# Optimization experiments

Measured on AMD Instinct MI355X. Metric: run time of the kernel, lower is better.

The kernel has to match this reference:

```python
import jax, jax.numpy as jnp
import numpy as np
import math

B, S, F, D = 8, 2048, 1024, 1024
NEG = -1e9


def setup_inputs() -> dict:
    key = jax.random.key(0)
    ks = jax.random.split(key, 5)
    x = jax.random.normal(ks[0], (B, S, F), dtype=jnp.float32)
    r_mat = jax.random.normal(ks[1], (B, S, S), dtype=jnp.float32)
    # shared causal attention mask [S, S] (1 = keep, 0 = masked)
    attn_mask = jnp.tril(jnp.ones((S, S), dtype=jnp.float32))
    # per-batch padding mask [B, 1, S]: last 128 tokens of half the batch padded
    pad = jnp.ones((B, 1, S), dtype=jnp.float32)
    pad = pad.at[B // 2:, :, S - 128:].set(0.0)
    Wq = jax.random.normal(ks[2], (F, D), dtype=jnp.float32) / math.sqrt(F)
    Wk = jax.random.normal(ks[3], (F, D), dtype=jnp.float32) / math.sqrt(F)
    Wv = jax.random.normal(ks[4], (F, D), dtype=jnp.float32) / math.sqrt(F)
    return {"x": x, "r_mat": r_mat, "attn_mask": attn_mask, "pad_mask": pad,
            "Wq": Wq, "Wk": Wk, "Wv": Wv}


def reference(x, r_mat, attn_mask, pad_mask, Wq, Wk, Wv):
    scale = math.sqrt(x.shape[-1])  # original scales by sqrt(features)
    q = jnp.einsum('bsf,fd->bsd', x, Wq)
    k = jnp.einsum('bsf,fd->bsd', x, Wk)
    v = jnp.einsum('bsf,fd->bsd', x, Wv)
    scores = jnp.einsum('bsd,btd->bst', q, k) / scale  # [B, S, S]
    keep = (pad_mask != 0.0) & (attn_mask[None] != 0.0)  # [B, S, S] broadcast
    r = jnp.where(keep, r_mat, NEG)
    r = jax.nn.softmax(r, axis=-1)
    scores = jnp.where(keep, scores + r, NEG)
    prob = jax.nn.softmax(scores, axis=-1)
    return jnp.einsum('bst,btd->bsd', prob, v)
```

## Files before the change

### kernel.cpp

```cpp
#include <hip/hip_runtime.h>
#include <hip/hip_bf16.h>

#define B_ 8
#define S_ 2048
#define F_ 1024
#define D_ 1024

typedef unsigned short u16;
typedef float f32x4 __attribute__((ext_vector_type(4)));
typedef __bf16 bf16x8 __attribute__((ext_vector_type(8)));
typedef unsigned short u16x8 __attribute__((ext_vector_type(8)));

__device__ __forceinline__ u16 f2bf(float f) {
  union { float f; unsigned u; } v; v.f = f;
  unsigned r = v.u + 0x7fff + ((v.u >> 16) & 1);
  return (u16)(r >> 16);
}
__device__ __forceinline__ float bf2f(u16 b) {
  union { unsigned u; float f; } v; v.u = ((unsigned)b) << 16;
  return v.f;
}

__device__ __forceinline__ void stage16(const u16* g, u16* l) {
  __builtin_amdgcn_global_load_lds(
      (const __attribute__((address_space(1))) void*)g,
      (__attribute__((address_space(3))) void*)l, 16, 0, 0);
}


__global__ void cast_x(const float* __restrict__ x, u16* __restrict__ xb, int n4) {
  int i = blockIdx.x * blockDim.x + threadIdx.x;
  int stride = gridDim.x * blockDim.x;
  for (; i < n4; i += stride) {
    float4 v = ((const float4*)x)[i];
    ushort4 o;
    o.x = f2bf(v.x); o.y = f2bf(v.y); o.z = f2bf(v.z); o.w = f2bf(v.w);
    ((ushort4*)xb)[i] = o;
  }
}

__global__ void transW(const float* __restrict__ Wq, const float* __restrict__ Wk,
                       const float* __restrict__ Wv, u16* __restrict__ Wt) {
  __shared__ float tile[32][33];
  int z = blockIdx.z;
  const float* W = (z == 0) ? Wq : ((z == 1) ? Wk : Wv);
  int f0 = blockIdx.y * 32, d0 = blockIdx.x * 32;
  int tx = threadIdx.x & 31, ty = threadIdx.x >> 5;
  for (int i = 0; i < 4; i++)
    tile[ty + i * 8][tx] = W[(size_t)(f0 + ty + i * 8) * D_ + d0 + tx];
  __syncthreads();
  u16* o = Wt + (size_t)z * D_ * F_;
  for (int i = 0; i < 4; i++)
    o[(size_t)(d0 + ty + i * 8) * F_ + f0 + tx] = f2bf(tile[tx][ty + i * 8]);
}

__global__ __launch_bounds__(256) void r_rowsum(const float* __restrict__ r,
                                                const float* __restrict__ pm,
                                                float* __restrict__ rs) {
  int row = blockIdx.x;
  int b = row >> 11, s = row & 2047;
  const float4* rp = (const float4*)(r + (size_t)row * S_);
  const float4* pp = (const float4*)(pm + (size_t)b * S_);
  int nv = (s >> 2) + 1;
  float acc = 0.f;
  for (int i = threadIdx.x; i < nv; i += 256) {
    float4 rv = rp[i];
    float4 pv = pp[i];
    int t0 = i << 2;
    #pragma unroll
    for (int j = 0; j < 4; j++) {
      int t = t0 + j;
      if (t <= s && (&pv.x)[j] != 0.f) acc += __expf((&rv.x)[j] - 16.f);
    }
  }
  for (int off = 1; off < 64; off <<= 1) acc += __shfl_xor(acc, off);
  __shared__ float wsum[4];
  int lane = threadIdx.x & 63, w = threadIdx.x >> 6;
  if (lane == 0) wsum[w] = acc;
  __syncthreads();
  if (threadIdx.x == 0) rs[row] = wsum[0] + wsum[1] + wsum[2] + wsum[3];
}


__device__ __forceinline__ void stageA(const u16* __restrict__ src, int ld, int h,
                                       u16* ldsA, int w, int l) {
  int base = ((w >> 2) * 128) + h * 64 + ((w & 3) * 16);
  int r = l >> 3, ch = (l & 7) ^ (l >> 3);
  #pragma unroll
  for (int i = 0; i < 2; i++) {
    int row = base + i * 8;
    stage16(src + (size_t)(row + r) * ld + ch * 8, ldsA + row * 64);
  }
}
__device__ __forceinline__ void stageB(const u16* __restrict__ src, int ld, int h,
                                       u16* ldsB, int w, int l) {
  int base = h * 128 + w * 16;
  int r = l >> 3, ch = (l & 7) ^ (l >> 3);
  #pragma unroll
  for (int i = 0; i < 2; i++) {
    int row = base + i * 8;
    stage16(src + (size_t)(row + r) * ld + ch * 8, ldsB + row * 64);
  }
}

__device__ __forceinline__ bf16x8 readfrag(const u16* lds, int row, int ks, int hi) {
  int c = ((ks << 6) + (hi << 4)) ^ ((row & 7) << 4);
  return *(const bf16x8*)((const char*)lds + row * 128 + c);
}

#define MFMA_QUAD(MB, KB)                                                        \
  __builtin_amdgcn_s_setprio(1);                                                 \
  _Pragma("unroll")                                                              \
  for (int m = 0; m < 4; m++)                                                    \
    _Pragma("unroll")                                                            \
    for (int n = 0; n < 4; n++)                                                  \
      acc[(MB) + m][n] = __builtin_amdgcn_mfma_f32_16x16x32_bf16(                \
          af[m], bfr[(KB) + n], acc[(MB) + m][n], 0, 0, 0);                      \
  __builtin_amdgcn_s_setprio(0);

#define SYNC_POINT()                                                             \
  __builtin_amdgcn_sched_barrier(0);                                             \
  __builtin_amdgcn_s_barrier();                                                  \
  __builtin_amdgcn_sched_barrier(0);

__device__ __forceinline__ void gemm256(const u16* __restrict__ A, int lda,
                                        const u16* __restrict__ B, int ldb,
                                        int nT, u16* lds, f32x4 acc[8][4]) {
  const int t = threadIdx.x, w = t >> 6, l = t & 63;
  const int wr = w >> 2, wc = w & 3;
  u16* A0 = lds;           u16* B0 = lds + 16384;
  u16* A1 = lds + 32768;   u16* B1 = lds + 49152;

  #pragma unroll
  for (int m = 0; m < 8; m++)
    #pragma unroll
    for (int n = 0; n < 4; n++)
      #pragma unroll
      for (int j = 0; j < 4; j++) acc[m][n][j] = 0.f;

  stageB(B, ldb, 0, B0, w, l);
  stageB(B, ldb, 1, B0, w, l);
  stageA(A, lda, 0, A0, w, l);
  stageA(A, lda, 1, A0, w, l);
  if (nT > 1) stageA(A + 64, lda, 0, A1, w, l);
  asm volatile("s_waitcnt vmcnt(4)" ::: "memory");
  SYNC_POINT()

  const int arow = wr * 128 + (l & 15), brow = wc * 64 + (l & 15), hi = l >> 4;

  for (int kt = 0; kt < nT; kt++) {
    u16* cA = (kt & 1) ? A1 : A0;
    u16* cB = (kt & 1) ? B1 : B0;
    u16* nA = (kt & 1) ? A0 : A1;
    u16* nB = (kt & 1) ? B0 : B1;
    const u16* An1 = A + (size_t)(kt + 1) * 64;
    const u16* Bn1 = B + (size_t)(kt + 1) * 64;
    const u16* An2 = A + (size_t)(kt + 2) * 64;
    const bool has1 = (kt + 1 < nT), has2 = (kt + 2 < nT);
    bf16x8 af[4], bfr[8];

    #pragma unroll
    for (int m = 0; m < 4; m++) af[m] = readfrag(cA, arow + m * 16, 0, hi);
    #pragma unroll
    for (int n = 0; n < 4; n++) bfr[n] = readfrag(cB, brow + n * 16, 0, hi);
    if (has1) stageB(Bn1, ldb, 0, nB, w, l);
    MFMA_QUAD(0, 0)

    #pragma unroll
    for (int m = 0; m < 4; m++) af[m] = readfrag(cA, arow + m * 16, 1, hi);
    #pragma unroll
    for (int n = 0; n < 4; n++) bfr[4 + n] = readfrag(cB, brow + n * 16, 1, hi);
    if (has1) {
      stageB(Bn1, ldb, 1, nB, w, l);
      asm volatile("s_waitcnt vmcnt(4)" ::: "memory");
    } else {
      asm volatile("s_waitcnt vmcnt(0)" ::: "memory");
    }
    SYNC_POINT()
    MFMA_QUAD(0, 4)

    #pragma unroll
    for (int m = 0; m < 4; m++) af[m] = readfrag(cA, arow + 64 + m * 16, 0, hi);
    if (has2) stageA(An2, lda, 0, cA, w, l);
    MFMA_QUAD(4, 0)

    #pragma unroll
    for (int m = 0; m < 4; m++) af[m] = readfrag(cA, arow + 64 + m * 16, 1, hi);
    if (has1) stageA(An1, lda, 1, nA, w, l);
    if (has1 && has2)  { asm volatile("s_waitcnt vmcnt(4)" ::: "memory"); }
    else if (has1)     { asm volatile("s_waitcnt vmcnt(2)" ::: "memory"); }
    else               { asm volatile("s_waitcnt vmcnt(0)" ::: "memory"); }
    SYNC_POINT()
    MFMA_QUAD(4, 4)
  }
}

__device__ __forceinline__ void store256_bf16(f32x4 acc[8][4], u16* smem,
                                              u16* dst, int ld) {
  int t = threadIdx.x, w = t >> 6, l = t & 63;
  int wr = w >> 2, wc = w & 3;
  #pragma unroll
  for (int q = 0; q < 4; q++) {
    __syncthreads();
    if (wr == (q >> 1)) {
      int mb = (q & 1) * 4;
      #pragma unroll
      for (int mm = 0; mm < 4; mm++)
        #pragma unroll
        for (int j = 0; j < 4; j++) {
          int row = mm * 16 + (l >> 4) * 4 + j;
          #pragma unroll
          for (int n = 0; n < 4; n++)
            smem[row * 264 + wc * 64 + n * 16 + (l & 15)] = f2bf(acc[mb + mm][n][j]);
        }
    }
    __syncthreads();
    #pragma unroll
    for (int i = 0; i < 4; i++) {
      int idx = i * 512 + t;
      int row = idx >> 5, ch = idx & 31;
      *(u16x8*)(dst + (size_t)(q * 64 + row) * ld + ch * 8) =
          *(const u16x8*)(smem + row * 264 + ch * 8);
    }
  }
}

__global__ __launch_bounds__(512, 2) void gemm_qkv(
    const u16* __restrict__ xb, const u16* __restrict__ Wt,
    u16* __restrict__ qb, u16* __restrict__ kb, u16* __restrict__ vT) {
  __shared__ __align__(16) u16 lds[65536];
  int z = blockIdx.z;
  f32x4 acc[8][4];
  if (z < 2) {
    int m0 = blockIdx.x * 256, n0 = blockIdx.y * 256;
    gemm256(xb + (size_t)m0 * F_, F_,
            Wt + (size_t)z * D_ * F_ + (size_t)n0 * F_, F_, F_ / 64, lds, acc);
    store256_bf16(acc, lds, ((z == 0) ? qb : kb) + (size_t)m0 * D_ + n0, D_);
  } else {
    int d0 = blockIdx.y * 256, s0g = blockIdx.x * 256;
    gemm256(Wt + 2ULL * D_ * F_ + (size_t)d0 * F_, F_,
            xb + (size_t)s0g * F_, F_, F_ / 64, lds, acc);
    int b = s0g >> 11, s0 = s0g & 2047;
    store256_bf16(acc, lds, vT + (size_t)b * D_ * S_ + (size_t)d0 * S_ + s0, S_);
  }
}

__global__ __launch_bounds__(512, 2) void attn_scores(
    const u16* __restrict__ qb, const u16* __restrict__ kb,
    const float* __restrict__ r_mat, const float* __restrict__ pm,
    const float* __restrict__ rs_r, u16* __restrict__ P,
    float* __restrict__ rowsum) {
  int mt = blockIdx.x, nt = blockIdx.y, b = blockIdx.z;
  if (nt > mt) return;
  __shared__ __align__(16) u16 lds[65536];
  int m0 = mt * 256, n0 = nt * 256;
  f32x4 acc[8][4];
  gemm256(qb + ((size_t)b * S_ + m0) * D_, D_,
          kb + ((size_t)b * S_ + n0) * D_, D_, D_ / 64, lds, acc);
  int t = threadIdx.x, w = t >> 6, l = t & 63;
  int wr = w >> 2, wc = w & 3;
  float* fs = (float*)lds;
  const float* rb = r_mat + (size_t)b * S_ * S_;
  const float* pmp = pm + (size_t)b * S_ + n0;
  #pragma unroll
  for (int q = 0; q < 4; q++) {
    __syncthreads();
    if (wr == (q >> 1)) {
      int mb = (q & 1) * 4;
      #pragma unroll
      for (int mm = 0; mm < 4; mm++)
        #pragma unroll
        for (int j = 0; j < 4; j++) {
          int row = mm * 16 + (l >> 4) * 4 + j;
          #pragma unroll
          for (int n = 0; n < 4; n++)
            fs[row * 260 + wc * 64 + n * 16 + (l & 15)] = acc[mb + mm][n][j];
        }
    }
    __syncthreads();
    int row = t >> 3, cg = t & 7;
    int srow = m0 + q * 64 + row;
    float invr = 1.f / rs_r[b * S_ + srow];
    const float* rrow = rb + (size_t)srow * S_ + n0 + cg * 32;
    u16* prow = P + (size_t)b * S_ * S_ + (size_t)srow * S_ + n0 + cg * 32;
    const float* fsc = fs + row * 260 + cg * 32;
    float rsum = 0.f;
    #pragma unroll
    for (int cc = 0; cc < 4; cc++) {
      int ch = (cg + cc) & 3;
      f32x4 q0 = *(const f32x4*)(fsc + ch * 8);
      f32x4 q1 = *(const f32x4*)(fsc + ch * 8 + 4);
      f32x4 r0 = *(const f32x4*)(rrow + ch * 8);
      f32x4 r1 = *(const f32x4*)(rrow + ch * 8 + 4);
      f32x4 p0 = *(const f32x4*)(pmp + cg * 32 + ch * 8);
      f32x4 p1 = *(const f32x4*)(pmp + cg * 32 + ch * 8 + 4);
      u16x8 o;
      #pragma unroll
      for (int k = 0; k < 8; k++) {
        int tc = n0 + cg * 32 + ch * 8 + k;
        float rv = (k < 4) ? r0[k] : r1[k - 4];
        float pmv = (k < 4) ? p0[k] : p1[k - 4];
        float qk = (k < 4) ? q0[k] : q1[k - 4];
        bool keep = (tc <= srow) && (pmv != 0.f);
        float rsm = __expf(rv - 16.f) * invr;
        float e = keep ? __expf(fmaf(qk, 0.03125f, rsm - 16.f)) : 0.f;
        u16 pb = f2bf(e); o[k] = pb; rsum += bf2f(pb);
      }
      *(u16x8*)(prow + ch * 8) = o;
    }
    for (int off = 1; off < 8; off <<= 1) rsum += __shfl_xor(rsum, off);
    if ((t & 7) == 0) atomicAdd(&rowsum[b * S_ + srow], rsum);
  }
}

__global__ __launch_bounds__(512, 2) void attn_pv(
    const u16* __restrict__ P, const u16* __restrict__ vT,
    const float* __restrict__ rowsum, float* __restrict__ out) {
  __shared__ __align__(16) u16 lds[65536];
  int mt = blockIdx.x, dt = blockIdx.y, b = blockIdx.z;
  int m0 = mt * 256, n0 = dt * 256;
  int kmax = m0 + 256;
  f32x4 acc[8][4];
  gemm256(P + ((size_t)b * S_ + m0) * S_, S_,
          vT + ((size_t)b * D_ + n0) * S_, S_, kmax / 64, lds, acc);
  int t = threadIdx.x, w = t >> 6, l = t & 63;
  int wr = w >> 2, wc = w & 3;
  float* fs = (float*)lds;
  #pragma unroll
  for (int q = 0; q < 4; q++) {
    __syncthreads();
    if (wr == (q >> 1)) {
      int mb = (q & 1) * 4;
      #pragma unroll
      for (int mm = 0; mm < 4; mm++)
        #pragma unroll
        for (int j = 0; j < 4; j++) {
          int row = mm * 16 + (l >> 4) * 4 + j;
          float inv = 1.f / rowsum[b * S_ + m0 + q * 64 + row];
          #pragma unroll
          for (int n = 0; n < 4; n++)
            fs[row * 260 + wc * 64 + n * 16 + (l & 15)] = acc[mb + mm][n][j] * inv;
        }
    }
    __syncthreads();
    #pragma unroll
    for (int i = 0; i < 8; i++) {
      int idx = i * 512 + t;
      int row = idx >> 6, c4 = (idx & 63) << 2;
      *(float4*)(out + ((size_t)b * S_ + m0 + q * 64 + row) * D_ + n0 + c4) =
          *(const float4*)(fs + row * 260 + c4);
    }
  }
}

extern "C" void kernel_launch(void* const* d_in, const int* in_sizes, int n_in,
                              void* d_out, int out_size, void* d_ws, size_t ws_size,
                              hipStream_t stream) {
  const float* x     = (const float*)d_in[0];
  const float* r_mat = (const float*)d_in[1];
  const float* pm    = (const float*)d_in[3];
  const float* Wq    = (const float*)d_in[4];
  const float* Wk    = (const float*)d_in[5];
  const float* Wv    = (const float*)d_in[6];
  float* out = (float*)d_out;
  char* ws = (char*)d_ws;

  u16*   qb     = (u16*)(ws + 0);
  u16*   kb     = (u16*)(ws + 33554432ULL);
  u16*   vT     = (u16*)(ws + 67108864ULL);
  float* rs_r   = (float*)(ws + 100663296ULL);
  float* rowsum = (float*)(ws + 100728832ULL);
  u16*   P      = (u16*)(ws + 100794368ULL);
  u16*   xb     = (u16*)(ws + 100794368ULL);
  u16*   Wt     = (u16*)(ws + 134348800ULL);

  cast_x<<<dim3(2048), dim3(256), 0, stream>>>(x, xb, (B_ * S_ * F_) / 4);
  transW<<<dim3(32, 32, 3), dim3(256), 0, stream>>>(Wq, Wk, Wv, Wt);
  r_rowsum<<<dim3(B_ * S_), dim3(256), 0, stream>>>(r_mat, pm, rs_r);
  gemm_qkv<<<dim3(64, 4, 3), dim3(512), 0, stream>>>(xb, Wt, qb, kb, vT);
  hipMemsetAsync(rowsum, 0, B_ * S_ * sizeof(float), stream);
  attn_scores<<<dim3(8, 8, 8), dim3(512), 0, stream>>>(qb, kb, r_mat, pm, rs_r, P, rowsum);
  attn_pv<<<dim3(8, 4, 8), dim3(512), 0, stream>>>(P, vT, rowsum, out);
}
```

Before: 306.7 us.

## Switch attention kernels to 128x128 tiles with triangular-only grid and heavy-first ordering

Adds a 128x128 GEMM core with 256 threads and uses it in attn_scores and attn_pv in place of the 256x256 tiles. attn_scores now launches only the lower-triangular tiles through a linear index decoded with sqrt, so no blocks exit early. Finer tiles cut wasted causal work on the diagonal and give more blocks per GPU. attn_pv is ordered so the longest rows start first. In exchange there is less operand reuse per tile and more global traffic and atomics.

```diff
diff --git a/kernel.cpp b/kernel.cpp
--- a/kernel.cpp
+++ b/kernel.cpp
@@ -82,6 +82,17 @@
 }
 
 
+__device__ __forceinline__ bf16x8 readfrag(const u16* lds, int row, int ks, int hi) {
+  int c = ((ks << 6) + (hi << 4)) ^ ((row & 7) << 4);
+  return *(const bf16x8*)((const char*)lds + row * 128 + c);
+}
+
+#define SYNC_POINT()                                                             \
+  __builtin_amdgcn_sched_barrier(0);                                             \
+  __builtin_amdgcn_s_barrier();                                                  \
+  __builtin_amdgcn_sched_barrier(0);
+
+
 __device__ __forceinline__ void stageA(const u16* __restrict__ src, int ld, int h,
                                        u16* ldsA, int w, int l) {
   int base = ((w >> 2) * 128) + h * 64 + ((w & 3) * 16);
@@ -101,11 +112,6 @@
     int row = base + i * 8;
     stage16(src + (size_t)(row + r) * ld + ch * 8, ldsB + row * 64);
   }
-}
-
-__device__ __forceinline__ bf16x8 readfrag(const u16* lds, int row, int ks, int hi) {
-  int c = ((ks << 6) + (hi << 4)) ^ ((row & 7) << 4);
-  return *(const bf16x8*)((const char*)lds + row * 128 + c);
 }
 
 #define MFMA_QUAD(MB, KB)                                                        \
@@ -117,11 +123,6 @@
       acc[(MB) + m][n] = __builtin_amdgcn_mfma_f32_16x16x32_bf16(                \
           af[m], bfr[(KB) + n], acc[(MB) + m][n], 0, 0, 0);                      \
   __builtin_amdgcn_s_setprio(0);
-
-#define SYNC_POINT()                                                             \
-  __builtin_amdgcn_sched_barrier(0);                                             \
-  __builtin_amdgcn_s_barrier();                                                  \
-  __builtin_amdgcn_sched_barrier(0);
 
 __device__ __forceinline__ void gemm256(const u16* __restrict__ A, int lda,
                                         const u16* __restrict__ B, int ldb,
@@ -245,45 +246,134 @@
   }
 }
 
-__global__ __launch_bounds__(512, 2) void attn_scores(
+
+__device__ __forceinline__ void stage128(const u16* __restrict__ src, int ld, int h,
+                                         u16* ldsT, int w, int l) {
+  int base = h * 64 + w * 16;
+  int r = l >> 3, ch = (l & 7) ^ (l >> 3);
+  #pragma unroll
+  for (int i = 0; i < 2; i++) {
+    int row = base + i * 8;
+    stage16(src + (size_t)(row + r) * ld + ch * 8, ldsT + row * 64);
+  }
+}
+
+#define MFMA16(AF, BF)                                                           \
+  __builtin_amdgcn_s_setprio(1);                                                 \
+  _Pragma("unroll")                                                              \
+  for (int m = 0; m < 4; m++)                                                    \
+    _Pragma("unroll")                                                            \
+    for (int n = 0; n < 4; n++)                                                  \
+      acc[m][n] = __builtin_amdgcn_mfma_f32_16x16x32_bf16(                       \
+          AF[m], BF[n], acc[m][n], 0, 0, 0);                                     \
+  __builtin_amdgcn_s_setprio(0);
+
+__device__ __forceinline__ void gemm128(const u16* __restrict__ A, int lda,
+                                        const u16* __restrict__ B, int ldb,
+                                        int nT, u16* lds, f32x4 acc[4][4]) {
+  const int t = threadIdx.x, w = t >> 6, l = t & 63;
+  const int wr = w >> 1, wc = w & 1;
+  u16* A0 = lds;          u16* B0 = lds + 8192;
+  u16* A1 = lds + 16384;  u16* B1 = lds + 24576;
+
+  #pragma unroll
+  for (int m = 0; m < 4; m++)
+    #pragma unroll
+    for (int n = 0; n < 4; n++)
+      #pragma unroll
+      for (int j = 0; j < 4; j++) acc[m][n][j] = 0.f;
+
+  stage128(A, lda, 0, A0, w, l);
+  stage128(A, lda, 1, A0, w, l);
+  stage128(B, ldb, 0, B0, w, l);
+  stage128(B, ldb, 1, B0, w, l);
+  if (nT > 1) {
+    stage128(A + 64, lda, 0, A1, w, l);
+    stage128(A + 64, lda, 1, A1, w, l);
+    asm volatile("s_waitcnt vmcnt(4)" ::: "memory");
+  } else {
+    asm volatile("s_waitcnt vmcnt(0)" ::: "memory");
+  }
+  SYNC_POINT()
+
+  const int arow = wr * 64 + (l & 15), brow = wc * 64 + (l & 15), hi = l >> 4;
+
+  for (int kt = 0; kt < nT; kt++) {
+    u16* cA = (kt & 1) ? A1 : A0;
+    u16* cB = (kt & 1) ? B1 : B0;
+    u16* nB = (kt & 1) ? B0 : B1;
+    const bool has1 = (kt + 1 < nT), has2 = (kt + 2 < nT);
+    bf16x8 a0f[4], b0f[4], a1f[4], b1f[4];
+
+    #pragma unroll
+    for (int m = 0; m < 4; m++) a0f[m] = readfrag(cA, arow + m * 16, 0, hi);
+    #pragma unroll
+    for (int n = 0; n < 4; n++) b0f[n] = readfrag(cB, brow + n * 16, 0, hi);
+    #pragma unroll
+    for (int m = 0; m < 4; m++) a1f[m] = readfrag(cA, arow + m * 16, 1, hi);
+    #pragma unroll
+    for (int n = 0; n < 4; n++) b1f[n] = readfrag(cB, brow + n * 16, 1, hi);
+    if (has1) {
+      stage128(B + (size_t)(kt + 1) * 64, ldb, 0, nB, w, l);
+      stage128(B + (size_t)(kt + 1) * 64, ldb, 1, nB, w, l);
+    }
+    MFMA16(a0f, b0f)
+    asm volatile("s_waitcnt lgkmcnt(0)" ::: "memory");
+    SYNC_POINT()
+
+    if (has2) {
+      stage128(A + (size_t)(kt + 2) * 64, lda, 0, cA, w, l);
+      stage128(A + (size_t)(kt + 2) * 64, lda, 1, cA, w, l);
+    }
+    MFMA16(a1f, b1f)
+    if (has2)      { asm volatile("s_waitcnt vmcnt(4)" ::: "memory"); }
+    else if (has1) { asm volatile("s_waitcnt vmcnt(0)" ::: "memory"); }
+    SYNC_POINT()
+  }
+}
+
+__global__ __launch_bounds__(256, 2) void attn_scores(
     const u16* __restrict__ qb, const u16* __restrict__ kb,
     const float* __restrict__ r_mat, const float* __restrict__ pm,
     const float* __restrict__ rs_r, u16* __restrict__ P,
     float* __restrict__ rowsum) {
-  int mt = blockIdx.x, nt = blockIdx.y, b = blockIdx.z;
-  if (nt > mt) return;
-  __shared__ __align__(16) u16 lds[65536];
-  int m0 = mt * 256, n0 = nt * 256;
-  f32x4 acc[8][4];
-  gemm256(qb + ((size_t)b * S_ + m0) * D_, D_,
+  __shared__ __align__(16) u16 lds[32768];
+  int b = blockIdx.y;
+  int x = blockIdx.x;
+  int mt = (int)((sqrtf(8.f * x + 1.f) - 1.f) * 0.5f);
+  while ((mt + 1) * (mt + 2) / 2 <= x) mt++;
+  while (mt * (mt + 1) / 2 > x) mt--;
+  int nt = x - mt * (mt + 1) / 2;
+  int m0 = mt * 128, n0 = nt * 128;
+  f32x4 acc[4][4];
+  gemm128(qb + ((size_t)b * S_ + m0) * D_, D_,
           kb + ((size_t)b * S_ + n0) * D_, D_, D_ / 64, lds, acc);
   int t = threadIdx.x, w = t >> 6, l = t & 63;
-  int wr = w >> 2, wc = w & 3;
+  int wr = w >> 1, wc = w & 1;
   float* fs = (float*)lds;
   const float* rb = r_mat + (size_t)b * S_ * S_;
   const float* pmp = pm + (size_t)b * S_ + n0;
   #pragma unroll
-  for (int q = 0; q < 4; q++) {
-    __syncthreads();
-    if (wr == (q >> 1)) {
-      int mb = (q & 1) * 4;
-      #pragma unroll
-      for (int mm = 0; mm < 4; mm++)
+  for (int h = 0; h < 2; h++) {
+    __syncthreads();
+    if (wr == h) {
+      #pragma unroll
+      for (int m = 0; m < 4; m++)
         #pragma unroll
         for (int j = 0; j < 4; j++) {
-          int row = mm * 16 + (l >> 4) * 4 + j;
+          int row = m * 16 + (l >> 4) * 4 + j;
           #pragma unroll
           for (int n = 0; n < 4; n++)
-            fs[row * 260 + wc * 64 + n * 16 + (l & 15)] = acc[mb + mm][n][j];
+            fs[row * 132 + wc * 64 + n * 16 + (l & 15)] = acc[m][n][j];
         }
     }
     __syncthreads();
-    int row = t >> 3, cg = t & 7;
-    int srow = m0 + q * 64 + row;
+    int row = t >> 2, cg = t & 3;
+    int srow = m0 + h * 64 + row;
     float invr = 1.f / rs_r[b * S_ + srow];
     const float* rrow = rb + (size_t)srow * S_ + n0 + cg * 32;
     u16* prow = P + (size_t)b * S_ * S_ + (size_t)srow * S_ + n0 + cg * 32;
-    const float* fsc = fs + row * 260 + cg * 32;
+    const float* fsc = fs + row * 132 + cg * 32;
     float rsum = 0.f;
     #pragma unroll
     for (int cc = 0; cc < 4; cc++) {
@@ -308,47 +398,47 @@
       }
       *(u16x8*)(prow + ch * 8) = o;
     }
-    for (int off = 1; off < 8; off <<= 1) rsum += __shfl_xor(rsum, off);
-    if ((t & 7) == 0) atomicAdd(&rowsum[b * S_ + srow], rsum);
-  }
-}
-
-__global__ __launch_bounds__(512, 2) void attn_pv(
+    rsum += __shfl_xor(rsum, 1);
+    rsum += __shfl_xor(rsum, 2);
+    if ((t & 3) == 0) atomicAdd(&rowsum[b * S_ + srow], rsum);
+  }
+}
+
+__global__ __launch_bounds__(256, 2) void attn_pv(
     const u16* __restrict__ P, const u16* __restrict__ vT,
     const float* __restrict__ rowsum, float* __restrict__ out) {
-  __shared__ __align__(16) u16 lds[65536];
-  int mt = blockIdx.x, dt = blockIdx.y, b = blockIdx.z;
-  int m0 = mt * 256, n0 = dt * 256;
-  int kmax = m0 + 256;
-  f32x4 acc[8][4];
-  gemm256(P + ((size_t)b * S_ + m0) * S_, S_,
-          vT + ((size_t)b * D_ + n0) * S_, S_, kmax / 64, lds, acc);
+  __shared__ __align__(16) u16 lds[32768];
+  int mt = 15 - blockIdx.x, dt = blockIdx.y, b = blockIdx.z;
+  int m0 = mt * 128, n0 = dt * 128;
+  int nT = (m0 + 128) / 64;
+  f32x4 acc[4][4];
+  gemm128(P + ((size_t)b * S_ + m0) * S_, S_,
+          vT + ((size_t)b * D_ + n0) * S_, S_, nT, lds, acc);
   int t = threadIdx.x, w = t >> 6, l = t & 63;
-  int wr = w >> 2, wc = w & 3;
+  int wr = w >> 1, wc = w & 1;
   float* fs = (float*)lds;
   #pragma unroll
-  for (int q = 0; q < 4; q++) {
-    __syncthreads();
-    if (wr == (q >> 1)) {
-      int mb = (q & 1) * 4;
-      #pragma unroll
-      for (int mm = 0; mm < 4; mm++)
+  for (int h = 0; h < 2; h++) {
+    __syncthreads();
+    if (wr == h) {
+      #pragma unroll
+      for (int m = 0; m < 4; m++)
         #pragma unroll
         for (int j = 0; j < 4; j++) {
-          int row = mm * 16 + (l >> 4) * 4 + j;
-          float inv = 1.f / rowsum[b * S_ + m0 + q * 64 + row];
+          int row = m * 16 + (l >> 4) * 4 + j;
+          float inv = 1.f / rowsum[b * S_ + m0 + h * 64 + row];
           #pragma unroll
           for (int n = 0; n < 4; n++)
-            fs[row * 260 + wc * 64 + n * 16 + (l & 15)] = acc[mb + mm][n][j] * inv;
+            fs[row * 132 + wc * 64 + n * 16 + (l & 15)] = acc[m][n][j] * inv;
         }
     }
     __syncthreads();
     #pragma unroll
     for (int i = 0; i < 8; i++) {
-      int idx = i * 512 + t;
-      int row = idx >> 6, c4 = (idx & 63) << 2;
-      *(float4*)(out + ((size_t)b * S_ + m0 + q * 64 + row) * D_ + n0 + c4) =
-          *(const float4*)(fs + row * 260 + c4);
+      int idx = i * 256 + t;
+      int row = idx >> 5, c4 = (idx & 31) << 2;
+      *(float4*)(out + ((size_t)b * S_ + m0 + h * 64 + row) * D_ + n0 + c4) =
+          *(const float4*)(fs + row * 132 + c4);
     }
   }
 }
@@ -379,6 +469,6 @@
   r_rowsum<<<dim3(B_ * S_), dim3(256), 0, stream>>>(r_mat, pm, rs_r);
   gemm_qkv<<<dim3(64, 4, 3), dim3(512), 0, stream>>>(xb, Wt, qb, kb, vT);
   hipMemsetAsync(rowsum, 0, B_ * S_ * sizeof(float), stream);
-  attn_scores<<<dim3(8, 8, 8), dim3(512), 0, stream>>>(qb, kb, r_mat, pm, rs_r, P, rowsum);
-  attn_pv<<<dim3(8, 4, 8), dim3(512), 0, stream>>>(P, vT, rowsum, out);
-}
+  attn_scores<<<dim3(136, 8), dim3(256), 0, stream>>>(qb, kb, r_mat, pm, rs_r, P, rowsum);
+  attn_pv<<<dim3(16, 8, 8), dim3(256), 0, stream>>>(P, vT, rowsum, out);
+}
```

Result: no change. 307.3 us (+0.2%).
